# Optimization experiments

Hardware: AMD Instinct MI355X
Metric: run time of the kernel (lower is better)

The kernel has to match this reference:

```python
import jax, jax.numpy as jnp
import numpy as np

LATENT = 128
N_NODES = 50000
N_EDGES = 800000
LN_EPS = 1e-5


def _glorot(key, fan_in, fan_out):
    lim = np.sqrt(6.0 / (fan_in + fan_out)).astype(np.float32)
    return jax.random.uniform(key, (fan_in, fan_out), jnp.float32, -lim, lim)


def setup_inputs() -> dict:
    key = jax.random.key(0)
    ks = jax.random.split(key, 10)
    node_latents = jax.random.normal(ks[0], (1, N_NODES, LATENT), jnp.float32)
    mesh_edge_latents = jax.random.normal(ks[1], (1, N_EDGES, LATENT), jnp.float32)
    senders = jax.random.randint(ks[2], (N_EDGES,), 0, N_NODES, jnp.int32)
    receivers = jax.random.randint(ks[3], (N_EDGES,), 0, N_NODES, jnp.int32)
    # mesh_edge_net: Linear(3L, L), ReLU, Linear(L, L), ReLU, LayerNorm(L)
    me_w1 = _glorot(ks[4], 3 * LATENT, LATENT)
    me_b1 = jnp.zeros((LATENT,), jnp.float32)
    me_w2 = _glorot(ks[5], LATENT, LATENT)
    me_b2 = jnp.zeros((LATENT,), jnp.float32)
    me_g = jnp.ones((LATENT,), jnp.float32)
    me_beta = jnp.zeros((LATENT,), jnp.float32)
    # node_feature_net: Linear(2L, L), ReLU, Linear(L, L), ReLU, LayerNorm(L)
    nf_w1 = _glorot(ks[6], 2 * LATENT, LATENT)
    nf_b1 = jnp.zeros((LATENT,), jnp.float32)
    nf_w2 = _glorot(ks[7], LATENT, LATENT)
    nf_b2 = jnp.zeros((LATENT,), jnp.float32)
    nf_g = jnp.ones((LATENT,), jnp.float32)
    nf_beta = jnp.zeros((LATENT,), jnp.float32)
    return dict(node_latents=node_latents, mesh_edge_latents=mesh_edge_latents,
                senders=senders, receivers=receivers,
                me_w1=me_w1, me_b1=me_b1, me_w2=me_w2, me_b2=me_b2, me_g=me_g, me_beta=me_beta,
                nf_w1=nf_w1, nf_b1=nf_b1, nf_w2=nf_w2, nf_b2=nf_b2, nf_g=nf_g, nf_beta=nf_beta)


def _mlp_ln(x, w1, b1, w2, b2, g, beta):
    h = jax.nn.relu(x @ w1 + b1)
    h = jax.nn.relu(h @ w2 + b2)
    mu = jnp.mean(h, axis=-1, keepdims=True)
    var = jnp.var(h, axis=-1, keepdims=True)
    return (h - mu) * jax.lax.rsqrt(var + LN_EPS) * g + beta


def reference(node_latents, mesh_edge_latents, senders, receivers,
              me_w1, me_b1, me_w2, me_b2, me_g, me_beta,
              nf_w1, nf_b1, nf_w2, nf_b2, nf_g, nf_beta):
    # gather sender/receiver node features: [B, E, L]
    edge_in = jnp.concatenate([node_latents[:, senders, :],
                               node_latents[:, receivers, :],
                               mesh_edge_latents], axis=-1)
    new_edges = _mlp_ln(edge_in, me_w1, me_b1, me_w2, me_b2, me_g, me_beta)
    # scatter_add messages to receiver nodes along dim=1
    aggr = jax.vmap(lambda e: jax.ops.segment_sum(e, receivers, num_segments=N_NODES))(new_edges)
    node_in = jnp.concatenate([node_latents, aggr], axis=-1)
    new_nodes = _mlp_ln(node_in, nf_w1, nf_b1, nf_w2, nf_b2, nf_g, nf_beta)
    new_nodes = new_nodes + node_latents  # residual
    new_edges = new_edges + mesh_edge_latents  # residual
    return new_nodes, new_edges
```

## Files before the change

kernel.cpp:

```cpp
#include <hip/hip_runtime.h>
#include <stdint.h>

typedef unsigned short u16;
typedef __bf16 bf16x8 __attribute__((ext_vector_type(8)));
typedef float f32x4 __attribute__((ext_vector_type(4)));

#define N_NODES 50000
#define N_EDGES 800000
#define NTILES  (N_EDGES / 64)
#define LN_EPS 1e-5f

__device__ __forceinline__ uint4 pack8(const float* __restrict__ p) {
    const float4 f0 = ((const float4*)p)[0];
    const float4 f1 = ((const float4*)p)[1];
    union { __bf16 b[8]; uint4 q; } t;
    t.b[0] = (__bf16)f0.x; t.b[1] = (__bf16)f0.y; t.b[2] = (__bf16)f0.z; t.b[3] = (__bf16)f0.w;
    t.b[4] = (__bf16)f1.x; t.b[5] = (__bf16)f1.y; t.b[6] = (__bf16)f1.z; t.b[7] = (__bf16)f1.w;
    return t.q;
}

__global__ void pack_weights(const float* __restrict__ w1e, const float* __restrict__ w2e,
                             const float* __restrict__ w1n, const float* __restrict__ w2n,
                             uint4* __restrict__ out)
{
    const int t = blockIdx.x * 256 + threadIdx.x;
    const float* W; int idx;
    if (t < 6144)       { W = w1e; idx = t; }
    else if (t < 8192)  { W = w2e; idx = t - 6144; }
    else if (t < 12288) { W = w1n; idx = t - 8192; }
    else                { W = w2n; idx = t - 12288; }
    const int lane = idx & 63;
    const int col16 = (idx >> 6) & 7;
    const int kb = idx >> 9;
    const int row0 = kb * 32 + (lane >> 4) * 8;
    const int col = col16 * 16 + (lane & 15);
    union { __bf16 b[8]; uint4 q; } v;
#pragma unroll
    for (int j = 0; j < 8; ++j) v.b[j] = (__bf16)W[(size_t)(row0 + j) * 128 + col];
    out[t] = v.q;
}

__global__ void convert_node(const float* __restrict__ node, uint4* __restrict__ node_bf) {
    const int idx = blockIdx.x * 256 + threadIdx.x;
    node_bf[idx] = pack8(node + (size_t)(idx >> 4) * 128 + (idx & 15) * 8);
}

__global__ void hist_kernel(const int* __restrict__ receivers, int* __restrict__ cnt) {
    const int e = blockIdx.x * 256 + threadIdx.x;
    if (e < N_EDGES) atomicAdd(&cnt[receivers[e]], 1);
}

#define SCAN_NB 196
__global__ void scan1(const int* __restrict__ cnt, int* __restrict__ bsum) {
    __shared__ int wsum[4];
    const int i = blockIdx.x * 256 + threadIdx.x;
    int v = (i < N_NODES) ? cnt[i] : 0;
#pragma unroll
    for (int off = 1; off < 64; off <<= 1) v += __shfl_xor(v, off, 64);
    if ((threadIdx.x & 63) == 0) wsum[threadIdx.x >> 6] = v;
    __syncthreads();
    if (threadIdx.x == 0) bsum[blockIdx.x] = wsum[0] + wsum[1] + wsum[2] + wsum[3];
}
__global__ void scan2(const int* __restrict__ bsum, int* __restrict__ boff) {
    __shared__ int s[256];
    const int t = threadIdx.x;
    const int v = (t < SCAN_NB) ? bsum[t] : 0;
    s[t] = v; __syncthreads();
    for (int off = 1; off < 256; off <<= 1) {
        const int u = (t >= off) ? s[t - off] : 0;
        __syncthreads(); s[t] += u; __syncthreads();
    }
    if (t < SCAN_NB) boff[t] = s[t] - v;
}
__global__ void scan3(const int* __restrict__ cnt, const int* __restrict__ boff,
                      int* __restrict__ cursor) {
    __shared__ int s[256];
    const int i = blockIdx.x * 256 + threadIdx.x;
    const int t = threadIdx.x;
    const int v = (i < N_NODES) ? cnt[i] : 0;
    s[t] = v; __syncthreads();
    for (int off = 1; off < 256; off <<= 1) {
        const int u = (t >= off) ? s[t - off] : 0;
        __syncthreads(); s[t] += u; __syncthreads();
    }
    if (i < N_NODES) cursor[i] = boff[blockIdx.x] + s[t] - v;
}

__global__ void scatter_kernel(const int* __restrict__ senders, const int* __restrict__ receivers,
                               int* __restrict__ cursor,
                               int* __restrict__ sorted_eid, int* __restrict__ pos_of,
                               int* __restrict__ snd_sorted, int* __restrict__ rcv_sorted) {
    const int e = blockIdx.x * 256 + threadIdx.x;
    if (e < N_EDGES) {
        const int rc = receivers[e];
        const int pos = atomicAdd(&cursor[rc], 1);
        sorted_eid[pos] = e;
        pos_of[e] = pos;
        snd_sorted[pos] = senders[e];
        rcv_sorted[pos] = rc;
    }
}

__global__ void permute_elat(const float* __restrict__ elat, const int* __restrict__ pos_of,
                             uint4* __restrict__ elat_s) {
    const int idx = blockIdx.x * 256 + threadIdx.x;
    const int e = idx >> 4, ch = idx & 15;
    const int p = pos_of[e];
    elat_s[(size_t)p * 16 + ch] = pack8(elat + (size_t)e * 128 + ch * 8);
}

template<int SORTED>
__global__ __launch_bounds__(256, 3)
void edge_mlp_kernel(const u16* __restrict__ node_bf, const float* __restrict__ elat,
                     const u16* __restrict__ elat_s,
                     const int* __restrict__ senders, const int* __restrict__ receivers,
                     const int* __restrict__ sorted_eid,
                     const int* __restrict__ snd_sorted, const int* __restrict__ rcv_sorted,
                     const float* __restrict__ b1, const float* __restrict__ b2,
                     const float* __restrict__ gam, const float* __restrict__ bet,
                     const uint4* __restrict__ w1p, const uint4* __restrict__ w2p,
                     float* __restrict__ eout, float* __restrict__ aggr)
{
    __shared__ __align__(16) u16 x_lds[3 * 64 * 128];
    __shared__ int rcv_s[64];
    __shared__ int eid_s[64];
    __shared__ float2 part[256];
    __shared__ float muv[64], rsv[64];

    float* lnf = (float*)x_lds;

    const int tid = threadIdx.x;
    const int w = tid >> 6;
    const int lane = tid & 63;
    const int cl = lane & 15;
    const int q = lane >> 4;
    const int n_base = w * 32;

    float b1v[2], b2v[2], gv[2], bv[2];
#pragma unroll
    for (int n = 0; n < 2; ++n) {
        const int c = n_base + n * 16 + cl;
        b1v[n] = b1[c]; b2v[n] = b2[c];
        gv[n]  = gam[c]; bv[n] = bet[c];
    }

    const int nchunk = gridDim.x;
    const int chunk = (blockIdx.x & 7) * (nchunk >> 3) + (blockIdx.x >> 3);
    const int t_lo = (int)(((long long)chunk * NTILES) / nchunk);
    const int t_hi = (int)(((long long)(chunk + 1) * NTILES) / nchunk);

    for (int tile = t_lo; tile < t_hi; ++tile) {
        const int base = tile * 64;

        {
            const int ch = tid & 15;
            const int r0 = tid >> 4;
#pragma unroll
            for (int gp = 0; gp < 4; ++gp) {
                const int row = gp * 16 + r0;
                const int rx = row & 7;
                const int p = base + row;
                int sn, rc, eid;
                if (SORTED) {
                    sn = snd_sorted[p]; rc = rcv_sorted[p]; eid = sorted_eid[p];
                } else {
                    sn = senders[p]; rc = receivers[p]; eid = p;
                }
                if (ch == 0) { rcv_s[row] = rc; eid_s[row] = eid; }
                uint4* dst = (uint4*)x_lds + row * 16;
                dst[ch ^ rx]          = ((const uint4*)(node_bf + (size_t)sn * 128))[ch];
                dst[1024 + (ch ^ rx)] = ((const uint4*)(node_bf + (size_t)rc * 128))[ch];
                if (SORTED)
                    dst[2048 + (ch ^ rx)] = ((const uint4*)(elat_s + (size_t)p * 128))[ch];
                else
                    dst[2048 + (ch ^ rx)] = pack8(elat + (size_t)p * 128 + ch * 8);
            }
        }
        __syncthreads();

        f32x4 acc[4][2];
#pragma unroll
        for (int m = 0; m < 4; ++m)
#pragma unroll
            for (int n = 0; n < 2; ++n)
#pragma unroll
                for (int r = 0; r < 4; ++r) acc[m][n][r] = 0.f;

        uint4 wreg[14][2];
#pragma unroll
        for (int kb = 0; kb < 2; ++kb)
#pragma unroll
            for (int n = 0; n < 2; ++n)
                wreg[kb][n] = w1p[(kb * 8 + w * 2 + n) * 64 + lane];

#pragma unroll
        for (int kb = 0; kb < 12; ++kb) {
            if (kb + 2 < 12) {
#pragma unroll
                for (int n = 0; n < 2; ++n)
                    wreg[kb + 2][n] = w1p[((kb + 2) * 8 + w * 2 + n) * 64 + lane];
            }
            const int p = kb >> 2, k2 = kb & 3;
            bf16x8 a[4];
#pragma unroll
            for (int m = 0; m < 4; ++m) {
                const int row = m * 16 + cl;
                a[m] = __builtin_bit_cast(bf16x8,
                    ((const uint4*)x_lds)[p * 1024 + row * 16 + ((k2 * 4 + q) ^ (row & 7))]);
            }
#pragma unroll
            for (int m = 0; m < 4; ++m)
#pragma unroll
                for (int n = 0; n < 2; ++n)
                    acc[m][n] = __builtin_amdgcn_mfma_f32_16x16x32_bf16(
                        a[m], __builtin_bit_cast(bf16x8, wreg[kb][n]), acc[m][n], 0, 0, 0);
        }

        uint4 w2reg[4][2];
#pragma unroll
        for (int kb = 0; kb < 4; ++kb)
#pragma unroll
            for (int n = 0; n < 2; ++n)
                w2reg[kb][n] = w2p[(kb * 8 + w * 2 + n) * 64 + lane];

        __syncthreads();

        {
            __bf16* hb = (__bf16*)x_lds;
#pragma unroll
            for (int m = 0; m < 4; ++m)
#pragma unroll
                for (int n = 0; n < 2; ++n)
#pragma unroll
                    for (int r = 0; r < 4; ++r) {
                        const int row = m * 16 + q * 4 + r;
                        const int col = n_base + n * 16 + cl;
                        hb[row * 128 + (((col >> 3) ^ (row & 7)) << 3) + (col & 7)] =
                            (__bf16)fmaxf(acc[m][n][r] + b1v[n], 0.f);
                    }
        }
        __syncthreads();

#pragma unroll
        for (int m = 0; m < 4; ++m)
#pragma unroll
            for (int n = 0; n < 2; ++n)
#pragma unroll
                for (int r = 0; r < 4; ++r) acc[m][n][r] = 0.f;
#pragma unroll
        for (int kb = 0; kb < 4; ++kb) {
            bf16x8 a[4];
#pragma unroll
            for (int m = 0; m < 4; ++m) {
                const int row = m * 16 + cl;
                a[m] = __builtin_bit_cast(bf16x8,
                    ((const uint4*)x_lds)[row * 16 + ((kb * 4 + q) ^ (row & 7))]);
            }
#pragma unroll
            for (int m = 0; m < 4; ++m)
#pragma unroll
                for (int n = 0; n < 2; ++n)
                    acc[m][n] = __builtin_amdgcn_mfma_f32_16x16x32_bf16(
                        a[m], __builtin_bit_cast(bf16x8, w2reg[kb][n]), acc[m][n], 0, 0, 0);
        }

#pragma unroll
        for (int m = 0; m < 4; ++m)
#pragma unroll
            for (int n = 0; n < 2; ++n)
#pragma unroll
                for (int r = 0; r < 4; ++r)
                    acc[m][n][r] = fmaxf(acc[m][n][r] + b2v[n], 0.f);

#pragma unroll
        for (int m = 0; m < 4; ++m)
#pragma unroll
            for (int r = 0; r < 4; ++r) {
                float s  = acc[m][0][r] + acc[m][1][r];
                float ss = acc[m][0][r] * acc[m][0][r] + acc[m][1][r] * acc[m][1][r];
#pragma unroll
                for (int off = 1; off < 16; off <<= 1) {
                    s  += __shfl_xor(s, off, 64);
                    ss += __shfl_xor(ss, off, 64);
                }
                if (cl == 0) part[w * 64 + m * 16 + q * 4 + r] = make_float2(s, ss);
            }
        __syncthreads();
        if (tid < 64) {
            float s = 0.f, ss = 0.f;
#pragma unroll
            for (int ww = 0; ww < 4; ++ww) { const float2 pp = part[ww * 64 + tid]; s += pp.x; ss += pp.y; }
            const float mu = s * (1.f / 128.f);
            const float var = ss * (1.f / 128.f) - mu * mu;
            muv[tid] = mu;
            rsv[tid] = rsqrtf(var + LN_EPS);
        }
        __syncthreads();

#pragma unroll
        for (int m = 0; m < 4; ++m)
#pragma unroll
            for (int r = 0; r < 4; ++r) {
                const int row = m * 16 + q * 4 + r;
                const float mu = muv[row];
                const float rs = rsv[row];
                float* orow = eout + (size_t)eid_s[row] * 128;
#pragma unroll
                for (int n = 0; n < 2; ++n) {
                    const int col = n_base + n * 16 + cl;
                    const float ln = (acc[m][n][r] - mu) * rs * gv[n] + bv[n];
                    lnf[row * 128 + col] = ln;
                    const float e = (float)((__bf16*)x_lds)[16384 + row * 128 + (((col >> 3) ^ (row & 7)) << 3) + (col & 7)];
                    orow[col] = ln + e;
                }
            }
        __syncthreads();

        {
            const int c = tid & 127;
            const int h = tid >> 7;
            const int rstart = h * 32, rend = rstart + 32;
            float sacc = 0.f; int flushed = 0;
#pragma unroll 1
            for (int r = rstart; r < rend; ++r) {
                sacc += lnf[r * 128 + c];
                const int rc = rcv_s[r];
                const bool last = (r == 63);
                const bool bnd = last || (rc != rcv_s[r + 1]);
                if (bnd) {
                    float* dst = &aggr[(size_t)rc * 128 + c];
                    if (SORTED && !last && flushed) *dst = sacc;
                    else atomicAdd(dst, sacc);
                    sacc = 0.f; flushed = 1;
                }
            }
            if (sacc != 0.f)
                atomicAdd(&aggr[(size_t)rcv_s[rend - 1] * 128 + c], sacc);
        }
        __syncthreads();
    }
}

__global__ __launch_bounds__(256, 4)
void node_mlp_kernel(const float* __restrict__ node, const float* __restrict__ aggr,
                     const float* __restrict__ b1, const float* __restrict__ b2,
                     const float* __restrict__ gam, const float* __restrict__ bet,
                     const uint4* __restrict__ w1p, const uint4* __restrict__ w2p,
                     float* __restrict__ nout)
{
    __shared__ __align__(16) u16 x_lds[2 * 64 * 128];
    __shared__ float2 part[256];
    __shared__ float muv[64], rsv[64];

    const int tid = threadIdx.x;
    const int w = tid >> 6;
    const int lane = tid & 63;
    const int cl = lane & 15;
    const int q = lane >> 4;
    const int n_base = w * 32;

    float b1v[2], b2v[2], gv[2], bv[2];
#pragma unroll
    for (int n = 0; n < 2; ++n) {
        const int c = n_base + n * 16 + cl;
        b1v[n] = b1[c]; b2v[n] = b2[c];
        gv[n]  = gam[c]; bv[n] = bet[c];
    }

    const int ntiles = (N_NODES + 63) / 64;
    for (int tile = blockIdx.x; tile < ntiles; tile += gridDim.x) {
        const int base = tile * 64;

        {
            const int ch = tid & 15;
            const int r0 = tid >> 4;
#pragma unroll
            for (int gp = 0; gp < 4; ++gp) {
                const int row = gp * 16 + r0;
                const int rx = row & 7;
                int gn = base + row;
                if (gn >= N_NODES) gn = N_NODES - 1;
                uint4* dst = (uint4*)x_lds + row * 16;
                dst[ch ^ rx]          = pack8(node + (size_t)gn * 128 + ch * 8);
                dst[1024 + (ch ^ rx)] = pack8(aggr + (size_t)gn * 128 + ch * 8);
            }
        }
        __syncthreads();

        f32x4 acc[4][2];
#pragma unroll
        for (int m = 0; m < 4; ++m)
#pragma unroll
            for (int n = 0; n < 2; ++n)
#pragma unroll
                for (int r = 0; r < 4; ++r) acc[m][n][r] = 0.f;

        uint4 wreg[10][2];
#pragma unroll
        for (int kb = 0; kb < 2; ++kb)
#pragma unroll
            for (int n = 0; n < 2; ++n)
                wreg[kb][n] = w1p[(kb * 8 + w * 2 + n) * 64 + lane];

#pragma unroll
        for (int kb = 0; kb < 8; ++kb) {
            if (kb + 2 < 8) {
#pragma unroll
                for (int n = 0; n < 2; ++n)
                    wreg[kb + 2][n] = w1p[((kb + 2) * 8 + w * 2 + n) * 64 + lane];
            }
            const int p = kb >> 2, k2 = kb & 3;
            bf16x8 a[4];
#pragma unroll
            for (int m = 0; m < 4; ++m) {
                const int row = m * 16 + cl;
                a[m] = __builtin_bit_cast(bf16x8,
                    ((const uint4*)x_lds)[p * 1024 + row * 16 + ((k2 * 4 + q) ^ (row & 7))]);
            }
#pragma unroll
            for (int m = 0; m < 4; ++m)
#pragma unroll
                for (int n = 0; n < 2; ++n)
                    acc[m][n] = __builtin_amdgcn_mfma_f32_16x16x32_bf16(
                        a[m], __builtin_bit_cast(bf16x8, wreg[kb][n]), acc[m][n], 0, 0, 0);
        }

        uint4 w2reg[4][2];
#pragma unroll
        for (int kb = 0; kb < 4; ++kb)
#pragma unroll
            for (int n = 0; n < 2; ++n)
                w2reg[kb][n] = w2p[(kb * 8 + w * 2 + n) * 64 + lane];

        __syncthreads();

        {
            __bf16* hb = (__bf16*)(x_lds + 8192);
#pragma unroll
            for (int m = 0; m < 4; ++m)
#pragma unroll
                for (int n = 0; n < 2; ++n)
#pragma unroll
                    for (int r = 0; r < 4; ++r) {
                        const int row = m * 16 + q * 4 + r;
                        const int col = n_base + n * 16 + cl;
                        hb[row * 128 + (((col >> 3) ^ (row & 7)) << 3) + (col & 7)] =
                            (__bf16)fmaxf(acc[m][n][r] + b1v[n], 0.f);
                    }
        }
        __syncthreads();

#pragma unroll
        for (int m = 0; m < 4; ++m)
#pragma unroll
            for (int n = 0; n < 2; ++n)
#pragma unroll
                for (int r = 0; r < 4; ++r) acc[m][n][r] = 0.f;
#pragma unroll
        for (int kb = 0; kb < 4; ++kb) {
            bf16x8 a[4];
#pragma unroll
            for (int m = 0; m < 4; ++m) {
                const int row = m * 16 + cl;
                a[m] = __builtin_bit_cast(bf16x8,
                    ((const uint4*)x_lds)[1024 + row * 16 + ((kb * 4 + q) ^ (row & 7))]);
            }
#pragma unroll
            for (int m = 0; m < 4; ++m)
#pragma unroll
                for (int n = 0; n < 2; ++n)
                    acc[m][n] = __builtin_amdgcn_mfma_f32_16x16x32_bf16(
                        a[m], __builtin_bit_cast(bf16x8, w2reg[kb][n]), acc[m][n], 0, 0, 0);
        }
#pragma unroll
        for (int m = 0; m < 4; ++m)
#pragma unroll
            for (int n = 0; n < 2; ++n)
#pragma unroll
                for (int r = 0; r < 4; ++r)
                    acc[m][n][r] = fmaxf(acc[m][n][r] + b2v[n], 0.f);

#pragma unroll
        for (int m = 0; m < 4; ++m)
#pragma unroll
            for (int r = 0; r < 4; ++r) {
                float s  = acc[m][0][r] + acc[m][1][r];
                float ss = acc[m][0][r] * acc[m][0][r] + acc[m][1][r] * acc[m][1][r];
#pragma unroll
                for (int off = 1; off < 16; off <<= 1) {
                    s  += __shfl_xor(s, off, 64);
                    ss += __shfl_xor(ss, off, 64);
                }
                if (cl == 0) part[w * 64 + m * 16 + q * 4 + r] = make_float2(s, ss);
            }
        __syncthreads();
        if (tid < 64) {
            float s = 0.f, ss = 0.f;
#pragma unroll
            for (int ww = 0; ww < 4; ++ww) { const float2 pp = part[ww * 64 + tid]; s += pp.x; ss += pp.y; }
            const float mu = s * (1.f / 128.f);
            const float var = ss * (1.f / 128.f) - mu * mu;
            muv[tid] = mu;
            rsv[tid] = rsqrtf(var + LN_EPS);
        }
        __syncthreads();

#pragma unroll
        for (int m = 0; m < 4; ++m)
#pragma unroll
            for (int r = 0; r < 4; ++r) {
                const int row = m * 16 + q * 4 + r;
                if (base + row < N_NODES) {
                    const float mu = muv[row];
                    const float rs = rsv[row];
                    float* orow = nout + (size_t)(base + row) * 128;
#pragma unroll
                    for (int n = 0; n < 2; ++n) {
                        const int col = n_base + n * 16 + cl;
                        const float ln = (acc[m][n][r] - mu) * rs * gv[n] + bv[n];
                        const float e = (float)((__bf16*)x_lds)[row * 128 + (((col >> 3) ^ (row & 7)) << 3) + (col & 7)];
                        orow[col] = ln + e;
                    }
                }
            }
        __syncthreads();
    }
}

extern "C" void kernel_launch(void* const* d_in, const int* in_sizes, int n_in,
                              void* d_out, int out_size, void* d_ws, size_t ws_size,
                              hipStream_t stream) {
    (void)in_sizes; (void)n_in; (void)out_size;
    const float* node = (const float*)d_in[0];
    const float* elat = (const float*)d_in[1];
    const int* senders = (const int*)d_in[2];
    const int* receivers = (const int*)d_in[3];
    const float* me_w1 = (const float*)d_in[4];
    const float* me_b1 = (const float*)d_in[5];
    const float* me_w2 = (const float*)d_in[6];
    const float* me_b2 = (const float*)d_in[7];
    const float* me_g  = (const float*)d_in[8];
    const float* me_be = (const float*)d_in[9];
    const float* nf_w1 = (const float*)d_in[10];
    const float* nf_b1 = (const float*)d_in[11];
    const float* nf_w2 = (const float*)d_in[12];
    const float* nf_b2 = (const float*)d_in[13];
    const float* nf_g  = (const float*)d_in[14];
    const float* nf_be = (const float*)d_in[15];

    float* out_nodes = (float*)d_out;
    float* out_edges = out_nodes + (size_t)N_NODES * 128;

    char* ob = (char*)d_out;
    u16* node_bf    = (u16*)ob;
    int* sorted_eid = (int*)(ob + 12800000);
    int* pos_of     = (int*)(ob + 16000000);
    int* snd_sorted = (int*)(ob + 19200000);
    int* rcv_sorted = (int*)(ob + 22400000);

    char* ws = (char*)d_ws;
    const size_t off_aggr   = 0;
    const size_t off_wpack  = off_aggr  + (size_t)N_NODES * 128 * sizeof(float);
    const size_t off_cnt    = off_wpack + 14336 * sizeof(uint4);
    const size_t off_cursor = off_cnt   + (size_t)N_NODES * sizeof(int);
    const size_t off_scan   = off_cursor+ (size_t)N_NODES * sizeof(int);
    const size_t off_elat_s = off_scan  + 4096;
    const size_t need_b     = off_cnt;
    const size_t need_a     = off_elat_s + (size_t)N_EDGES * 128 * sizeof(u16);
    if (ws_size < need_b) return;

    float* aggr   = (float*)(ws + off_aggr);
    uint4* wpack  = (uint4*)(ws + off_wpack);
    int*   cnt    = (int*)(ws + off_cnt);
    int*   cursor = (int*)(ws + off_cursor);
    int*   bsum   = (int*)(ws + off_scan);
    int*   boff   = (int*)(ws + off_scan + 2048);
    u16*   elat_s = (u16*)(ws + off_elat_s);
    const bool tier_a = (ws_size >= need_a);

    hipMemsetAsync(aggr, 0, (size_t)N_NODES * 128 * sizeof(float), stream);
    pack_weights<<<56, 256, 0, stream>>>(me_w1, me_w2, nf_w1, nf_w2, wpack);
    convert_node<<<3125, 256, 0, stream>>>(node, (uint4*)node_bf);

    if (tier_a) {
        hipMemsetAsync(cnt, 0, (size_t)N_NODES * sizeof(int), stream);
        hist_kernel<<<(N_EDGES + 255) / 256, 256, 0, stream>>>(receivers, cnt);
        scan1<<<SCAN_NB, 256, 0, stream>>>(cnt, bsum);
        scan2<<<1, 256, 0, stream>>>(bsum, boff);
        scan3<<<SCAN_NB, 256, 0, stream>>>(cnt, boff, cursor);
        scatter_kernel<<<(N_EDGES + 255) / 256, 256, 0, stream>>>(
            senders, receivers, cursor, sorted_eid, pos_of, snd_sorted, rcv_sorted);
        permute_elat<<<50000, 256, 0, stream>>>(elat, pos_of, (uint4*)elat_s);
        edge_mlp_kernel<1><<<768, 256, 0, stream>>>(node_bf, elat, elat_s,
                                                    senders, receivers,
                                                    sorted_eid, snd_sorted, rcv_sorted,
                                                    me_b1, me_b2, me_g, me_be,
                                                    wpack, wpack + 6144,
                                                    out_edges, aggr);
    } else {
        edge_mlp_kernel<0><<<768, 256, 0, stream>>>(node_bf, elat, elat_s,
                                                    senders, receivers,
                                                    sorted_eid, snd_sorted, rcv_sorted,
                                                    me_b1, me_b2, me_g, me_be,
                                                    wpack, wpack + 6144,
                                                    out_edges, aggr);
    }
    node_mlp_kernel<<<782, 256, 0, stream>>>(node, aggr,
                                             nf_b1, nf_b2, nf_g, nf_be,
                                             wpack + 8192, wpack + 12288,
                                             out_nodes);
}
```

Baseline: 1.117 ms.

## Pre-gather sender rows into an interleaved sorted edge buffer before the GEMM

Adds a build_x_snd pass that gathers sender node rows in receiver-sorted order into a combined per-edge buffer X, stored next to the permuted bf16 edge latents. The edge GEMM then reads sender and edge-latent data with contiguous loads, and sender/receiver indices are packed into one int2 array. The intent is to take the random sender gather off the GEMM kernel's critical path. In exchange it adds a separate kernel that writes and re-reads 256 bytes per edge, and needs a larger workspace (512 bytes per edge). The fallback path is split out as a separate non-templated fused kernel.

```diff
diff --git a/kernel.cpp b/kernel.cpp
--- a/kernel.cpp
+++ b/kernel.cpp
@@ -89,37 +89,39 @@
 __global__ void scatter_kernel(const int* __restrict__ senders, const int* __restrict__ receivers,
                                int* __restrict__ cursor,
                                int* __restrict__ sorted_eid, int* __restrict__ pos_of,
-                               int* __restrict__ snd_sorted, int* __restrict__ rcv_sorted) {
+                               int2* __restrict__ sr_sorted) {
     const int e = blockIdx.x * 256 + threadIdx.x;
     if (e < N_EDGES) {
         const int rc = receivers[e];
         const int pos = atomicAdd(&cursor[rc], 1);
         sorted_eid[pos] = e;
         pos_of[e] = pos;
-        snd_sorted[pos] = senders[e];
-        rcv_sorted[pos] = rc;
-    }
-}
-
-__global__ void permute_elat(const float* __restrict__ elat, const int* __restrict__ pos_of,
-                             uint4* __restrict__ elat_s) {
+        sr_sorted[pos] = make_int2(senders[e], rc);
+    }
+}
+
+__global__ void build_x_elat(const float* __restrict__ elat, const int* __restrict__ pos_of,
+                             uint4* __restrict__ X) {
     const int idx = blockIdx.x * 256 + threadIdx.x;
     const int e = idx >> 4, ch = idx & 15;
     const int p = pos_of[e];
-    elat_s[(size_t)p * 16 + ch] = pack8(elat + (size_t)e * 128 + ch * 8);
-}
-
-template<int SORTED>
+    X[(size_t)p * 32 + 16 + ch] = pack8(elat + (size_t)e * 128 + ch * 8);
+}
+__global__ void build_x_snd(const u16* __restrict__ node_bf, const int2* __restrict__ sr_sorted,
+                            uint4* __restrict__ X) {
+    const int idx = blockIdx.x * 256 + threadIdx.x;
+    const int p = idx >> 4, ch = idx & 15;
+    const int sn = sr_sorted[p].x;
+    X[(size_t)p * 32 + ch] = ((const uint4*)(node_bf + (size_t)sn * 128))[ch];
+}
+
 __global__ __launch_bounds__(256, 3)
-void edge_mlp_kernel(const u16* __restrict__ node_bf, const float* __restrict__ elat,
-                     const u16* __restrict__ elat_s,
-                     const int* __restrict__ senders, const int* __restrict__ receivers,
-                     const int* __restrict__ sorted_eid,
-                     const int* __restrict__ snd_sorted, const int* __restrict__ rcv_sorted,
-                     const float* __restrict__ b1, const float* __restrict__ b2,
-                     const float* __restrict__ gam, const float* __restrict__ bet,
-                     const uint4* __restrict__ w1p, const uint4* __restrict__ w2p,
-                     float* __restrict__ eout, float* __restrict__ aggr)
+void edge_gemm(const u16* __restrict__ node_bf, const uint4* __restrict__ X,
+               const int* __restrict__ sorted_eid, const int2* __restrict__ sr_sorted,
+               const float* __restrict__ b1, const float* __restrict__ b2,
+               const float* __restrict__ gam, const float* __restrict__ bet,
+               const uint4* __restrict__ w1p, const uint4* __restrict__ w2p,
+               float* __restrict__ eout, float* __restrict__ aggr)
 {
     __shared__ __align__(16) u16 x_lds[3 * 64 * 128];
     __shared__ int rcv_s[64];
@@ -160,20 +162,12 @@
                 const int row = gp * 16 + r0;
                 const int rx = row & 7;
                 const int p = base + row;
-                int sn, rc, eid;
-                if (SORTED) {
-                    sn = snd_sorted[p]; rc = rcv_sorted[p]; eid = sorted_eid[p];
-                } else {
-                    sn = senders[p]; rc = receivers[p]; eid = p;
-                }
-                if (ch == 0) { rcv_s[row] = rc; eid_s[row] = eid; }
+                const int2 sr = sr_sorted[p];
+                if (ch == 0) { rcv_s[row] = sr.y; eid_s[row] = sorted_eid[p]; }
                 uint4* dst = (uint4*)x_lds + row * 16;
-                dst[ch ^ rx]          = ((const uint4*)(node_bf + (size_t)sn * 128))[ch];
-                dst[1024 + (ch ^ rx)] = ((const uint4*)(node_bf + (size_t)rc * 128))[ch];
-                if (SORTED)
-                    dst[2048 + (ch ^ rx)] = ((const uint4*)(elat_s + (size_t)p * 128))[ch];
-                else
-                    dst[2048 + (ch ^ rx)] = pack8(elat + (size_t)p * 128 + ch * 8);
+                dst[ch ^ rx]          = X[(size_t)p * 32 + ch];
+                dst[1024 + (ch ^ rx)] = ((const uint4*)(node_bf + (size_t)sr.y * 128))[ch];
+                dst[2048 + (ch ^ rx)] = X[(size_t)p * 32 + 16 + ch];
             }
         }
         __syncthreads();
@@ -329,10 +323,206 @@
                 const bool bnd = last || (rc != rcv_s[r + 1]);
                 if (bnd) {
                     float* dst = &aggr[(size_t)rc * 128 + c];
-                    if (SORTED && !last && flushed) *dst = sacc;
+                    if (!last && flushed) *dst = sacc;
                     else atomicAdd(dst, sacc);
                     sacc = 0.f; flushed = 1;
                 }
+            }
+            if (sacc != 0.f)
+                atomicAdd(&aggr[(size_t)rcv_s[rend - 1] * 128 + c], sacc);
+        }
+        __syncthreads();
+    }
+}
+
+__global__ __launch_bounds__(256, 3)
+void edge_fused(const u16* __restrict__ node_bf, const float* __restrict__ elat,
+                const int* __restrict__ senders, const int* __restrict__ receivers,
+                const float* __restrict__ b1, const float* __restrict__ b2,
+                const float* __restrict__ gam, const float* __restrict__ bet,
+                const uint4* __restrict__ w1p, const uint4* __restrict__ w2p,
+                float* __restrict__ eout, float* __restrict__ aggr)
+{
+    __shared__ __align__(16) u16 x_lds[3 * 64 * 128];
+    __shared__ int rcv_s[64];
+    __shared__ float2 part[256];
+    __shared__ float muv[64], rsv[64];
+    float* lnf = (float*)x_lds;
+
+    const int tid = threadIdx.x;
+    const int w = tid >> 6;
+    const int lane = tid & 63;
+    const int cl = lane & 15;
+    const int q = lane >> 4;
+    const int n_base = w * 32;
+
+    float b1v[2], b2v[2], gv[2], bv[2];
+#pragma unroll
+    for (int n = 0; n < 2; ++n) {
+        const int c = n_base + n * 16 + cl;
+        b1v[n] = b1[c]; b2v[n] = b2[c];
+        gv[n]  = gam[c]; bv[n] = bet[c];
+    }
+
+    for (int tile = blockIdx.x; tile < NTILES; tile += gridDim.x) {
+        const int base = tile * 64;
+        {
+            const int ch = tid & 15;
+            const int r0 = tid >> 4;
+#pragma unroll
+            for (int gp = 0; gp < 4; ++gp) {
+                const int row = gp * 16 + r0;
+                const int rx = row & 7;
+                const int p = base + row;
+                const int sn = senders[p];
+                const int rc = receivers[p];
+                if (ch == 0) rcv_s[row] = rc;
+                uint4* dst = (uint4*)x_lds + row * 16;
+                dst[ch ^ rx]          = ((const uint4*)(node_bf + (size_t)sn * 128))[ch];
+                dst[1024 + (ch ^ rx)] = ((const uint4*)(node_bf + (size_t)rc * 128))[ch];
+                dst[2048 + (ch ^ rx)] = pack8(elat + (size_t)p * 128 + ch * 8);
+            }
+        }
+        __syncthreads();
+
+        f32x4 acc[4][2];
+#pragma unroll
+        for (int m = 0; m < 4; ++m)
+#pragma unroll
+            for (int n = 0; n < 2; ++n)
+#pragma unroll
+                for (int r = 0; r < 4; ++r) acc[m][n][r] = 0.f;
+        uint4 wreg[14][2];
+#pragma unroll
+        for (int kb = 0; kb < 2; ++kb)
+#pragma unroll
+            for (int n = 0; n < 2; ++n)
+                wreg[kb][n] = w1p[(kb * 8 + w * 2 + n) * 64 + lane];
+#pragma unroll
+        for (int kb = 0; kb < 12; ++kb) {
+            if (kb + 2 < 12) {
+#pragma unroll
+                for (int n = 0; n < 2; ++n)
+                    wreg[kb + 2][n] = w1p[((kb + 2) * 8 + w * 2 + n) * 64 + lane];
+            }
+            const int p = kb >> 2, k2 = kb & 3;
+            bf16x8 a[4];
+#pragma unroll
+            for (int m = 0; m < 4; ++m) {
+                const int row = m * 16 + cl;
+                a[m] = __builtin_bit_cast(bf16x8,
+                    ((const uint4*)x_lds)[p * 1024 + row * 16 + ((k2 * 4 + q) ^ (row & 7))]);
+            }
+#pragma unroll
+            for (int m = 0; m < 4; ++m)
+#pragma unroll
+                for (int n = 0; n < 2; ++n)
+                    acc[m][n] = __builtin_amdgcn_mfma_f32_16x16x32_bf16(
+                        a[m], __builtin_bit_cast(bf16x8, wreg[kb][n]), acc[m][n], 0, 0, 0);
+        }
+        uint4 w2reg[4][2];
+#pragma unroll
+        for (int kb = 0; kb < 4; ++kb)
+#pragma unroll
+            for (int n = 0; n < 2; ++n)
+                w2reg[kb][n] = w2p[(kb * 8 + w * 2 + n) * 64 + lane];
+        __syncthreads();
+        {
+            __bf16* hb = (__bf16*)x_lds;
+#pragma unroll
+            for (int m = 0; m < 4; ++m)
+#pragma unroll
+                for (int n = 0; n < 2; ++n)
+#pragma unroll
+                    for (int r = 0; r < 4; ++r) {
+                        const int row = m * 16 + q * 4 + r;
+                        const int col = n_base + n * 16 + cl;
+                        hb[row * 128 + (((col >> 3) ^ (row & 7)) << 3) + (col & 7)] =
+                            (__bf16)fmaxf(acc[m][n][r] + b1v[n], 0.f);
+                    }
+        }
+        __syncthreads();
+#pragma unroll
+        for (int m = 0; m < 4; ++m)
+#pragma unroll
+            for (int n = 0; n < 2; ++n)
+#pragma unroll
+                for (int r = 0; r < 4; ++r) acc[m][n][r] = 0.f;
+#pragma unroll
+        for (int kb = 0; kb < 4; ++kb) {
+            bf16x8 a[4];
+#pragma unroll
+            for (int m = 0; m < 4; ++m) {
+                const int row = m * 16 + cl;
+                a[m] = __builtin_bit_cast(bf16x8,
+                    ((const uint4*)x_lds)[row * 16 + ((kb * 4 + q) ^ (row & 7))]);
+            }
+#pragma unroll
+            for (int m = 0; m < 4; ++m)
+#pragma unroll
+                for (int n = 0; n < 2; ++n)
+                    acc[m][n] = __builtin_amdgcn_mfma_f32_16x16x32_bf16(
+                        a[m], __builtin_bit_cast(bf16x8, w2reg[kb][n]), acc[m][n], 0, 0, 0);
+        }
+#pragma unroll
+        for (int m = 0; m < 4; ++m)
+#pragma unroll
+            for (int n = 0; n < 2; ++n)
+#pragma unroll
+                for (int r = 0; r < 4; ++r)
+                    acc[m][n][r] = fmaxf(acc[m][n][r] + b2v[n], 0.f);
+#pragma unroll
+        for (int m = 0; m < 4; ++m)
+#pragma unroll
+            for (int r = 0; r < 4; ++r) {
+                float s  = acc[m][0][r] + acc[m][1][r];
+                float ss = acc[m][0][r] * acc[m][0][r] + acc[m][1][r] * acc[m][1][r];
+#pragma unroll
+                for (int off = 1; off < 16; off <<= 1) {
+                    s  += __shfl_xor(s, off, 64);
+                    ss += __shfl_xor(ss, off, 64);
+                }
+                if (cl == 0) part[w * 64 + m * 16 + q * 4 + r] = make_float2(s, ss);
+            }
+        __syncthreads();
+        if (tid < 64) {
+            float s = 0.f, ss = 0.f;
+#pragma unroll
+            for (int ww = 0; ww < 4; ++ww) { const float2 pp = part[ww * 64 + tid]; s += pp.x; ss += pp.y; }
+            const float mu = s * (1.f / 128.f);
+            const float var = ss * (1.f / 128.f) - mu * mu;
+            muv[tid] = mu;
+            rsv[tid] = rsqrtf(var + LN_EPS);
+        }
+        __syncthreads();
+#pragma unroll
+        for (int m = 0; m < 4; ++m)
+#pragma unroll
+            for (int r = 0; r < 4; ++r) {
+                const int row = m * 16 + q * 4 + r;
+                const float mu = muv[row];
+                const float rs = rsv[row];
+                float* orow = eout + (size_t)(base + row) * 128;
+#pragma unroll
+                for (int n = 0; n < 2; ++n) {
+                    const int col = n_base + n * 16 + cl;
+                    const float ln = (acc[m][n][r] - mu) * rs * gv[n] + bv[n];
+                    lnf[row * 128 + col] = ln;
+                    const float e = (float)((__bf16*)x_lds)[16384 + row * 128 + (((col >> 3) ^ (row & 7)) << 3) + (col & 7)];
+                    orow[col] = ln + e;
+                }
+            }
+        __syncthreads();
+        {
+            const int c = tid & 127;
+            const int h = tid >> 7;
+            const int rstart = h * 32, rend = rstart + 32;
+            float sacc = 0.f;
+#pragma unroll 1
+            for (int r = rstart; r < rend; ++r) {
+                sacc += lnf[r * 128 + c];
+                const bool bnd = (r == 63) || (rcv_s[r] != rcv_s[r + 1]);
+                if (bnd) { atomicAdd(&aggr[(size_t)rcv_s[r] * 128 + c], sacc); sacc = 0.f; }
             }
             if (sacc != 0.f)
                 atomicAdd(&aggr[(size_t)rcv_s[rend - 1] * 128 + c], sacc);
@@ -370,7 +560,6 @@
     const int ntiles = (N_NODES + 63) / 64;
     for (int tile = blockIdx.x; tile < ntiles; tile += gridDim.x) {
         const int base = tile * 64;
-
         {
             const int ch = tid & 15;
             const int r0 = tid >> 4;
@@ -394,14 +583,12 @@
             for (int n = 0; n < 2; ++n)
 #pragma unroll
                 for (int r = 0; r < 4; ++r) acc[m][n][r] = 0.f;
-
         uint4 wreg[10][2];
 #pragma unroll
         for (int kb = 0; kb < 2; ++kb)
 #pragma unroll
             for (int n = 0; n < 2; ++n)
                 wreg[kb][n] = w1p[(kb * 8 + w * 2 + n) * 64 + lane];
-
 #pragma unroll
         for (int kb = 0; kb < 8; ++kb) {
             if (kb + 2 < 8) {
@@ -424,16 +611,13 @@
                     acc[m][n] = __builtin_amdgcn_mfma_f32_16x16x32_bf16(
                         a[m], __builtin_bit_cast(bf16x8, wreg[kb][n]), acc[m][n], 0, 0, 0);
         }
-
         uint4 w2reg[4][2];
 #pragma unroll
         for (int kb = 0; kb < 4; ++kb)
 #pragma unroll
             for (int n = 0; n < 2; ++n)
                 w2reg[kb][n] = w2p[(kb * 8 + w * 2 + n) * 64 + lane];
-
-        __syncthreads();
-
+        __syncthreads();
         {
             __bf16* hb = (__bf16*)(x_lds + 8192);
 #pragma unroll
@@ -449,7 +633,6 @@
                     }
         }
         __syncthreads();
-
 #pragma unroll
         for (int m = 0; m < 4; ++m)
 #pragma unroll
@@ -479,7 +662,6 @@
 #pragma unroll
                 for (int r = 0; r < 4; ++r)
                     acc[m][n][r] = fmaxf(acc[m][n][r] + b2v[n], 0.f);
-
 #pragma unroll
         for (int m = 0; m < 4; ++m)
 #pragma unroll
@@ -504,7 +686,6 @@
             rsv[tid] = rsqrtf(var + LN_EPS);
         }
         __syncthreads();
-
 #pragma unroll
         for (int m = 0; m < 4; ++m)
 #pragma unroll
@@ -552,11 +733,10 @@
     float* out_edges = out_nodes + (size_t)N_NODES * 128;
 
     char* ob = (char*)d_out;
-    u16* node_bf    = (u16*)ob;
-    int* sorted_eid = (int*)(ob + 12800000);
-    int* pos_of     = (int*)(ob + 16000000);
-    int* snd_sorted = (int*)(ob + 19200000);
-    int* rcv_sorted = (int*)(ob + 22400000);
+    u16*  node_bf    = (u16*)ob;
+    int*  sorted_eid = (int*)(ob + 12800000);
+    int*  pos_of     = (int*)(ob + 16000000);
+    int2* sr_sorted  = (int2*)(ob + 19200000);
 
     char* ws = (char*)d_ws;
     const size_t off_aggr   = 0;
@@ -564,9 +744,9 @@
     const size_t off_cnt    = off_wpack + 14336 * sizeof(uint4);
     const size_t off_cursor = off_cnt   + (size_t)N_NODES * sizeof(int);
     const size_t off_scan   = off_cursor+ (size_t)N_NODES * sizeof(int);
-    const size_t off_elat_s = off_scan  + 4096;
+    const size_t off_X      = off_scan  + 4096;
     const size_t need_b     = off_cnt;
-    const size_t need_a     = off_elat_s + (size_t)N_EDGES * 128 * sizeof(u16);
+    const size_t need_s     = off_X + (size_t)N_EDGES * 512;
     if (ws_size < need_b) return;
 
     float* aggr   = (float*)(ws + off_aggr);
@@ -575,35 +755,32 @@
     int*   cursor = (int*)(ws + off_cursor);
     int*   bsum   = (int*)(ws + off_scan);
     int*   boff   = (int*)(ws + off_scan + 2048);
-    u16*   elat_s = (u16*)(ws + off_elat_s);
-    const bool tier_a = (ws_size >= need_a);
+    uint4* X      = (uint4*)(ws + off_X);
+    const bool tier_s = (ws_size >= need_s);
 
     hipMemsetAsync(aggr, 0, (size_t)N_NODES * 128 * sizeof(float), stream);
     pack_weights<<<56, 256, 0, stream>>>(me_w1, me_w2, nf_w1, nf_w2, wpack);
     convert_node<<<3125, 256, 0, stream>>>(node, (uint4*)node_bf);
 
-    if (tier_a) {
+    if (tier_s) {
         hipMemsetAsync(cnt, 0, (size_t)N_NODES * sizeof(int), stream);
         hist_kernel<<<(N_EDGES + 255) / 256, 256, 0, stream>>>(receivers, cnt);
         scan1<<<SCAN_NB, 256, 0, stream>>>(cnt, bsum);
         scan2<<<1, 256, 0, stream>>>(bsum, boff);
         scan3<<<SCAN_NB, 256, 0, stream>>>(cnt, boff, cursor);
         scatter_kernel<<<(N_EDGES + 255) / 256, 256, 0, stream>>>(
-            senders, receivers, cursor, sorted_eid, pos_of, snd_sorted, rcv_sorted);
-        permute_elat<<<50000, 256, 0, stream>>>(elat, pos_of, (uint4*)elat_s);
-        edge_mlp_kernel<1><<<768, 256, 0, stream>>>(node_bf, elat, elat_s,
-                                                    senders, receivers,
-                                                    sorted_eid, snd_sorted, rcv_sorted,
-                                                    me_b1, me_b2, me_g, me_be,
-                                                    wpack, wpack + 6144,
-                                                    out_edges, aggr);
+            senders, receivers, cursor, sorted_eid, pos_of, sr_sorted);
+        build_x_elat<<<50000, 256, 0, stream>>>(elat, pos_of, X);
+        build_x_snd<<<50000, 256, 0, stream>>>(node_bf, sr_sorted, X);
+        edge_gemm<<<768, 256, 0, stream>>>(node_bf, X, sorted_eid, sr_sorted,
+                                           me_b1, me_b2, me_g, me_be,
+                                           wpack, wpack + 6144,
+                                           out_edges, aggr);
     } else {
-        edge_mlp_kernel<0><<<768, 256, 0, stream>>>(node_bf, elat, elat_s,
-                                                    senders, receivers,
-                                                    sorted_eid, snd_sorted, rcv_sorted,
-                                                    me_b1, me_b2, me_g, me_be,
-                                                    wpack, wpack + 6144,
-                                                    out_edges, aggr);
+        edge_fused<<<768, 256, 0, stream>>>(node_bf, elat, senders, receivers,
+                                            me_b1, me_b2, me_g, me_be,
+                                            wpack, wpack + 6144,
+                                            out_edges, aggr);
     }
     node_mlp_kernel<<<782, 256, 0, stream>>>(node, aggr,
                                              nf_b1, nf_b2, nf_g, nf_be,
```

Measured after the change: 1.223 ms. +9.4%, slower.
